# Kernel tuning notes

Hardware: AMD Instinct MI355X
Metric: run time of the kernel (lower is better)

The kernel has to match this reference:

```python
import jax, jax.numpy as jnp
import numpy as np

N_FILTER = 32
NCENTS = 1024
BETA = 0.25  # commitment cost


def setup_inputs() -> dict:
    key = jax.random.key(0)
    k1, k2 = jax.random.split(key)
    lat = jax.random.normal(k1, (2048, 2048), dtype=jnp.float32)
    centroids = jax.random.normal(k2, (NCENTS, N_FILTER), dtype=jnp.float32)
    leak_factor = jnp.ones((), dtype=jnp.float32)
    return {"lat": lat, "centroids": centroids, "leak_factor": leak_factor}


def _vq(z, centroids):
    # z: [B, L, D]; centroids: [K, D]
    zf = z.reshape(-1, z.shape[-1])  # [N, D]
    # squared distances: ||z||^2 - 2 z.c + ||c||^2  -> [N, K]
    d = (jnp.sum(zf * zf, axis=1, keepdims=True)
         - 2.0 * zf @ centroids.T
         + jnp.sum(centroids * centroids, axis=1)[None, :])
    idx = jnp.argmin(d, axis=1)  # [N]
    zq = centroids[idx]  # gather, [N, D]
    sg = jax.lax.stop_gradient
    # VQ-VAE codebook + commitment losses
    loss = jnp.mean((sg(zf) - zq) ** 2) + BETA * jnp.mean((zf - sg(zq)) ** 2)
    # straight-through estimator
    zq_st = zf + sg(zq - zf)
    return zq_st.reshape(z.shape), loss


def reference(lat, centroids, leak_factor):
    B = lat.shape[0]
    lat_size = lat.shape[1]
    z = lat.reshape(B, lat_size // N_FILTER, N_FILTER)
    _zq, cent_loss = _vq(z, centroids)
    # NOTE: original forward overwrites the quantized result with raw lat
    new_lat = lat.reshape(B, lat_size)
    lf = jnp.clip(leak_factor, 0.001, 1000.0)
    return new_lat * lf, cent_loss
```

## Files before the change

### kernel.cpp

```cpp
#include <hip/hip_runtime.h>

#define D 32
#define K 1024
#define N_ROWS 131072
#define TOTAL_ELEMS 4194304
#define LOSS_SCALE (1.25f / 4194304.0f)

typedef __attribute__((ext_vector_type(8))) short short8;
typedef __attribute__((ext_vector_type(4))) float f32x4;

__device__ __forceinline__ unsigned short f2bf(float f) {
  unsigned u = __builtin_bit_cast(unsigned, f);
  unsigned r = u + 0x7FFFu + ((u >> 16) & 1u);
  return (unsigned short)(r >> 16);
}

__global__ __launch_bounds__(256) void prep_kernel(
    const float* __restrict__ cent, unsigned short* __restrict__ centbf,
    float4* __restrict__ cnormb4, float* __restrict__ loss_out) {
  int t = blockIdx.x * 256 + threadIdx.x;
  centbf[t] = f2bf(-2.0f * cent[t]);
  if (t == 0) *loss_out = 0.0f;
  if (t < K) {
    const float* c = cent + t * D;
    float s0 = 0.f, s1 = 0.f, s2 = 0.f, s3 = 0.f;
#pragma unroll
    for (int d = 0; d < D; d += 4) {
      s0 = fmaf(c[d], c[d], s0);
      s1 = fmaf(c[d + 1], c[d + 1], s1);
      s2 = fmaf(c[d + 2], c[d + 2], s2);
      s3 = fmaf(c[d + 3], c[d + 3], s3);
    }
    float cn = (s0 + s1) + (s2 + s3);
    cnormb4[t] = make_float4(cn, cn, cn, cn);
  }
}

__global__ __launch_bounds__(512) void vq_kernel(
    const float* __restrict__ lat, const unsigned short* __restrict__ centbf,
    const float4* __restrict__ cnormb4, const float* __restrict__ lf_ptr,
    float* __restrict__ out, float* __restrict__ loss_out) {
  __shared__ short8 sB8[4096];
  __shared__ f32x4 sCn4[1024];
  const int tid = threadIdx.x;
  const int lane = tid & 63;
  const int wave = tid >> 6;
  const int quad = lane >> 4;
  const int col  = lane & 15;
  const int rowbase = blockIdx.x * 256 + wave * 32;

  {
    const short8* gB8 = (const short8*)centbf;
#pragma unroll
    for (int j = 0; j < 8; ++j) sB8[j * 512 + tid] = gB8[j * 512 + tid];
    const uint4* g4 = (const uint4*)cnormb4;
    uint4* s4 = (uint4*)sCn4;
    s4[tid] = g4[tid];
    s4[512 + tid] = g4[512 + tid];
  }

  float lf = fminf(fmaxf(lf_ptr[0], 0.001f), 1000.0f);
  short8 a0, a1;
  float zz;
  {
    const float* p0 = lat + (size_t)(rowbase + col) * D + quad * 8;
    const float* p1 = p0 + 16 * D;
    float4 u0 = ((const float4*)p0)[0], u1 = ((const float4*)p0)[1];
    float4 w0 = ((const float4*)p1)[0], w1 = ((const float4*)p1)[1];
    a0[0] = (short)f2bf(u0.x); a0[1] = (short)f2bf(u0.y);
    a0[2] = (short)f2bf(u0.z); a0[3] = (short)f2bf(u0.w);
    a0[4] = (short)f2bf(u1.x); a0[5] = (short)f2bf(u1.y);
    a0[6] = (short)f2bf(u1.z); a0[7] = (short)f2bf(u1.w);
    a1[0] = (short)f2bf(w0.x); a1[1] = (short)f2bf(w0.y);
    a1[2] = (short)f2bf(w0.z); a1[3] = (short)f2bf(w0.w);
    a1[4] = (short)f2bf(w1.x); a1[5] = (short)f2bf(w1.y);
    a1[6] = (short)f2bf(w1.z); a1[7] = (short)f2bf(w1.w);
    float t0 = fmaf(u0.x, u0.x, fmaf(u0.y, u0.y, fmaf(u0.z, u0.z, u0.w * u0.w)));
    float t1 = fmaf(u1.x, u1.x, fmaf(u1.y, u1.y, fmaf(u1.z, u1.z, u1.w * u1.w)));
    float t2 = fmaf(w0.x, w0.x, fmaf(w0.y, w0.y, fmaf(w0.z, w0.z, w0.w * w0.w)));
    float t3 = fmaf(w1.x, w1.x, fmaf(w1.y, w1.y, fmaf(w1.z, w1.z, w1.w * w1.w)));
    zz = (t0 + t1) + (t2 + t3);
    float* o0 = out + (size_t)(rowbase + col) * D + quad * 8;
    float* o1 = o0 + 16 * D;
    float4 s00 = {u0.x * lf, u0.y * lf, u0.z * lf, u0.w * lf};
    float4 s01 = {u1.x * lf, u1.y * lf, u1.z * lf, u1.w * lf};
    float4 s10 = {w0.x * lf, w0.y * lf, w0.z * lf, w0.w * lf};
    float4 s11 = {w1.x * lf, w1.y * lf, w1.z * lf, w1.w * lf};
    ((float4*)o0)[0] = s00;
    ((float4*)o0)[1] = s01;
    ((float4*)o1)[0] = s10;
    ((float4*)o1)[1] = s11;
  }
  __syncthreads();

  const float INF = 3.4e38f;
  float m0[4] = {INF, INF, INF, INF};
  float m1[4] = {INF, INF, INF, INF};
  const int boff = col * 4 + quad;

#pragma unroll 8
  for (int f = 0; f < 64; ++f) {
    short8 b = sB8[f * 64 + boff];
    f32x4 c4 = sCn4[f * 16 + col];
    f32x4 d0 = __builtin_amdgcn_mfma_f32_16x16x32_bf16(a0, b, c4, 0, 0, 0);
    f32x4 d1 = __builtin_amdgcn_mfma_f32_16x16x32_bf16(a1, b, c4, 0, 0, 0);
#pragma unroll
    for (int r = 0; r < 4; ++r) {
      m0[r] = fminf(m0[r], d0[r]);
      m1[r] = fminf(m1[r], d1[r]);
    }
  }

#pragma unroll
  for (int off = 1; off < 16; off <<= 1) {
#pragma unroll
    for (int r = 0; r < 4; ++r) {
      m0[r] = fminf(m0[r], __shfl_xor(m0[r], off));
      m1[r] = fminf(m1[r], __shfl_xor(m1[r], off));
    }
  }

  float s = ((m0[0] + m0[1]) + (m0[2] + m0[3])) +
            ((m1[0] + m1[1]) + (m1[2] + m1[3]));
  s += __shfl_xor(s, 16);
  s += __shfl_xor(s, 32);

  zz += __shfl_xor(zz, 1);
  zz += __shfl_xor(zz, 2);
  zz += __shfl_xor(zz, 4);
  zz += __shfl_xor(zz, 8);
  zz += __shfl_xor(zz, 16);
  zz += __shfl_xor(zz, 32);

  float total = s + zz;
  __syncthreads();
  float* wsum = (float*)sB8;
  if (lane == 0) wsum[wave] = total;
  __syncthreads();
  if (tid == 0) {
    float blk = ((wsum[0] + wsum[1]) + (wsum[2] + wsum[3])) +
                ((wsum[4] + wsum[5]) + (wsum[6] + wsum[7]));
    atomicAdd(loss_out, blk * LOSS_SCALE);
  }
}

extern "C" void kernel_launch(void* const* d_in, const int* in_sizes, int n_in,
                              void* d_out, int out_size, void* d_ws, size_t ws_size,
                              hipStream_t stream) {
  const float* lat  = (const float*)d_in[0];
  const float* cent = (const float*)d_in[1];
  const float* lf   = (const float*)d_in[2];
  float* out = (float*)d_out;
  unsigned short* centbf = (unsigned short*)d_ws;
  float4* cnormb4 = (float4*)((char*)d_ws + 65536);
  float* loss = out + TOTAL_ELEMS;

  prep_kernel<<<K * D / 256, 256, 0, stream>>>(cent, centbf, cnormb4, loss);
  vq_kernel<<<N_ROWS / 256, 512, 0, stream>>>(lat, centbf, cnormb4, lf,
                                              out, loss);
}
```

Baseline: 88.90 us.

## Give each wave 64 rows and pre-swizzle the bf16 codebook layout

The VQ kernel drops from 512 to 256 threads per block. Each wave now owns 64 rows, so every codebook fragment read from LDS feeds four MFMAs instead of two. The prep kernel writes the bf16 centroids in fragment order with 16-byte vector stores, so the main loop indexes LDS directly by lane and the strided boff pattern goes away. The aim is fewer LDS reads per MFMA and cheaper codebook prep, at the cost of more registers and half as many waves per block to hide global-memory latency.

```diff
diff --git a/kernel.cpp b/kernel.cpp
--- a/kernel.cpp
+++ b/kernel.cpp
@@ -19,8 +19,23 @@
     const float* __restrict__ cent, unsigned short* __restrict__ centbf,
     float4* __restrict__ cnormb4, float* __restrict__ loss_out) {
   int t = blockIdx.x * 256 + threadIdx.x;
-  centbf[t] = f2bf(-2.0f * cent[t]);
   if (t == 0) *loss_out = 0.0f;
+  {
+    int f = t >> 6;
+    int rem = t & 63;
+    int q = rem >> 4;
+    int c = rem & 15;
+    int k0 = f * 16 + c;
+    const float* src = cent + k0 * D + q * 8;
+    float4 u0 = ((const float4*)src)[0];
+    float4 u1 = ((const float4*)src)[1];
+    short8 ch;
+    ch[0] = (short)f2bf(-2.0f * u0.x); ch[1] = (short)f2bf(-2.0f * u0.y);
+    ch[2] = (short)f2bf(-2.0f * u0.z); ch[3] = (short)f2bf(-2.0f * u0.w);
+    ch[4] = (short)f2bf(-2.0f * u1.x); ch[5] = (short)f2bf(-2.0f * u1.y);
+    ch[6] = (short)f2bf(-2.0f * u1.z); ch[7] = (short)f2bf(-2.0f * u1.w);
+    ((short8*)centbf)[t] = ch;
+  }
   if (t < K) {
     const float* c = cent + t * D;
     float s0 = 0.f, s1 = 0.f, s2 = 0.f, s3 = 0.f;
@@ -36,7 +51,7 @@
   }
 }
 
-__global__ __launch_bounds__(512) void vq_kernel(
+__global__ __launch_bounds__(256) void vq_kernel(
     const float* __restrict__ lat, const unsigned short* __restrict__ centbf,
     const float4* __restrict__ cnormb4, const float* __restrict__ lf_ptr,
     float* __restrict__ out, float* __restrict__ loss_out) {
@@ -47,67 +62,60 @@
   const int wave = tid >> 6;
   const int quad = lane >> 4;
   const int col  = lane & 15;
-  const int rowbase = blockIdx.x * 256 + wave * 32;
+  const int rowbase = blockIdx.x * 256 + wave * 64;
 
   {
     const short8* gB8 = (const short8*)centbf;
 #pragma unroll
-    for (int j = 0; j < 8; ++j) sB8[j * 512 + tid] = gB8[j * 512 + tid];
+    for (int j = 0; j < 16; ++j) sB8[j * 256 + tid] = gB8[j * 256 + tid];
     const uint4* g4 = (const uint4*)cnormb4;
     uint4* s4 = (uint4*)sCn4;
-    s4[tid] = g4[tid];
-    s4[512 + tid] = g4[512 + tid];
+#pragma unroll
+    for (int j = 0; j < 4; ++j) s4[j * 256 + tid] = g4[j * 256 + tid];
   }
 
   float lf = fminf(fmaxf(lf_ptr[0], 0.001f), 1000.0f);
-  short8 a0, a1;
-  float zz;
-  {
-    const float* p0 = lat + (size_t)(rowbase + col) * D + quad * 8;
-    const float* p1 = p0 + 16 * D;
-    float4 u0 = ((const float4*)p0)[0], u1 = ((const float4*)p0)[1];
-    float4 w0 = ((const float4*)p1)[0], w1 = ((const float4*)p1)[1];
-    a0[0] = (short)f2bf(u0.x); a0[1] = (short)f2bf(u0.y);
-    a0[2] = (short)f2bf(u0.z); a0[3] = (short)f2bf(u0.w);
-    a0[4] = (short)f2bf(u1.x); a0[5] = (short)f2bf(u1.y);
-    a0[6] = (short)f2bf(u1.z); a0[7] = (short)f2bf(u1.w);
-    a1[0] = (short)f2bf(w0.x); a1[1] = (short)f2bf(w0.y);
-    a1[2] = (short)f2bf(w0.z); a1[3] = (short)f2bf(w0.w);
-    a1[4] = (short)f2bf(w1.x); a1[5] = (short)f2bf(w1.y);
-    a1[6] = (short)f2bf(w1.z); a1[7] = (short)f2bf(w1.w);
+  short8 a[4];
+  float zz = 0.0f;
+#pragma unroll
+  for (int t = 0; t < 4; ++t) {
+    const float* p = lat + (size_t)(rowbase + t * 16 + col) * D + quad * 8;
+    float4 u0 = ((const float4*)p)[0], u1 = ((const float4*)p)[1];
+    a[t][0] = (short)f2bf(u0.x); a[t][1] = (short)f2bf(u0.y);
+    a[t][2] = (short)f2bf(u0.z); a[t][3] = (short)f2bf(u0.w);
+    a[t][4] = (short)f2bf(u1.x); a[t][5] = (short)f2bf(u1.y);
+    a[t][6] = (short)f2bf(u1.z); a[t][7] = (short)f2bf(u1.w);
     float t0 = fmaf(u0.x, u0.x, fmaf(u0.y, u0.y, fmaf(u0.z, u0.z, u0.w * u0.w)));
     float t1 = fmaf(u1.x, u1.x, fmaf(u1.y, u1.y, fmaf(u1.z, u1.z, u1.w * u1.w)));
-    float t2 = fmaf(w0.x, w0.x, fmaf(w0.y, w0.y, fmaf(w0.z, w0.z, w0.w * w0.w)));
-    float t3 = fmaf(w1.x, w1.x, fmaf(w1.y, w1.y, fmaf(w1.z, w1.z, w1.w * w1.w)));
-    zz = (t0 + t1) + (t2 + t3);
-    float* o0 = out + (size_t)(rowbase + col) * D + quad * 8;
-    float* o1 = o0 + 16 * D;
-    float4 s00 = {u0.x * lf, u0.y * lf, u0.z * lf, u0.w * lf};
-    float4 s01 = {u1.x * lf, u1.y * lf, u1.z * lf, u1.w * lf};
-    float4 s10 = {w0.x * lf, w0.y * lf, w0.z * lf, w0.w * lf};
-    float4 s11 = {w1.x * lf, w1.y * lf, w1.z * lf, w1.w * lf};
-    ((float4*)o0)[0] = s00;
-    ((float4*)o0)[1] = s01;
-    ((float4*)o1)[0] = s10;
-    ((float4*)o1)[1] = s11;
+    zz += t0 + t1;
+    float* o = out + (size_t)(rowbase + t * 16 + col) * D + quad * 8;
+    float4 s0 = {u0.x * lf, u0.y * lf, u0.z * lf, u0.w * lf};
+    float4 s1 = {u1.x * lf, u1.y * lf, u1.z * lf, u1.w * lf};
+    ((float4*)o)[0] = s0;
+    ((float4*)o)[1] = s1;
   }
   __syncthreads();
 
   const float INF = 3.4e38f;
   float m0[4] = {INF, INF, INF, INF};
   float m1[4] = {INF, INF, INF, INF};
-  const int boff = col * 4 + quad;
+  float m2[4] = {INF, INF, INF, INF};
+  float m3[4] = {INF, INF, INF, INF};
 
-#pragma unroll 8
+#pragma unroll 4
   for (int f = 0; f < 64; ++f) {
-    short8 b = sB8[f * 64 + boff];
+    short8 b = sB8[f * 64 + lane];
     f32x4 c4 = sCn4[f * 16 + col];
-    f32x4 d0 = __builtin_amdgcn_mfma_f32_16x16x32_bf16(a0, b, c4, 0, 0, 0);
-    f32x4 d1 = __builtin_amdgcn_mfma_f32_16x16x32_bf16(a1, b, c4, 0, 0, 0);
+    f32x4 d0 = __builtin_amdgcn_mfma_f32_16x16x32_bf16(a[0], b, c4, 0, 0, 0);
+    f32x4 d1 = __builtin_amdgcn_mfma_f32_16x16x32_bf16(a[1], b, c4, 0, 0, 0);
+    f32x4 d2 = __builtin_amdgcn_mfma_f32_16x16x32_bf16(a[2], b, c4, 0, 0, 0);
+    f32x4 d3 = __builtin_amdgcn_mfma_f32_16x16x32_bf16(a[3], b, c4, 0, 0, 0);
 #pragma unroll
     for (int r = 0; r < 4; ++r) {
       m0[r] = fminf(m0[r], d0[r]);
       m1[r] = fminf(m1[r], d1[r]);
+      m2[r] = fminf(m2[r], d2[r]);
+      m3[r] = fminf(m3[r], d3[r]);
     }
   }
 
@@ -117,11 +125,15 @@
     for (int r = 0; r < 4; ++r) {
       m0[r] = fminf(m0[r], __shfl_xor(m0[r], off));
       m1[r] = fminf(m1[r], __shfl_xor(m1[r], off));
+      m2[r] = fminf(m2[r], __shfl_xor(m2[r], off));
+      m3[r] = fminf(m3[r], __shfl_xor(m3[r], off));
     }
   }
 
-  float s = ((m0[0] + m0[1]) + (m0[2] + m0[3])) +
-            ((m1[0] + m1[1]) + (m1[2] + m1[3]));
+  float s = (((m0[0] + m0[1]) + (m0[2] + m0[3])) +
+             ((m1[0] + m1[1]) + (m1[2] + m1[3]))) +
+            (((m2[0] + m2[1]) + (m2[2] + m2[3])) +
+             ((m3[0] + m3[1]) + (m3[2] + m3[3])));
   s += __shfl_xor(s, 16);
   s += __shfl_xor(s, 32);
 
@@ -138,8 +150,7 @@
   if (lane == 0) wsum[wave] = total;
   __syncthreads();
   if (tid == 0) {
-    float blk = ((wsum[0] + wsum[1]) + (wsum[2] + wsum[3])) +
-                ((wsum[4] + wsum[5]) + (wsum[6] + wsum[7]));
+    float blk = (wsum[0] + wsum[1]) + (wsum[2] + wsum[3]);
     atomicAdd(loss_out, blk * LOSS_SCALE);
   }
 }
@@ -155,7 +166,7 @@
   float4* cnormb4 = (float4*)((char*)d_ws + 65536);
   float* loss = out + TOTAL_ELEMS;
 
-  prep_kernel<<<K * D / 256, 256, 0, stream>>>(cent, centbf, cnormb4, loss);
-  vq_kernel<<<N_ROWS / 256, 512, 0, stream>>>(lat, centbf, cnormb4, lf,
+  prep_kernel<<<K * D / 8 / 256, 256, 0, stream>>>(cent, centbf, cnormb4, loss);
+  vq_kernel<<<N_ROWS / 256, 256, 0, stream>>>(lat, centbf, cnormb4, lf,
                                               out, loss);
 }
```

After: 89.12 us. No clear change (+0.2%).
